# Kernel tuning notes

Measured on AMD Instinct MI355X. Metric: run time of the kernel, lower is better.

Reference implementation:

```python
import jax, jax.numpy as jnp
import numpy as np

B, S, H = 512, 200, 256

def setup_inputs() -> dict:
    key = jax.random.key(0)
    ks = jax.random.split(key, 7)
    scale = 1.0 / np.sqrt(H)
    return {
        "all_memory": jax.random.normal(ks[0], (B, S, H), dtype=jnp.float32),
        "last_memory": jax.random.normal(ks[1], (B, H), dtype=jnp.float32),
        "U": jax.random.normal(ks[2], (H, H), dtype=jnp.float32) * scale,   # U_meta weight
        "W": jax.random.normal(ks[3], (H, H), dtype=jnp.float32) * scale,   # W_meta weight
        "V": jax.random.normal(ks[4], (H, 1), dtype=jnp.float32) * scale,   # V_meta weight (stored as [H,1])
        "MetaW": jax.random.normal(ks[5], (4, H), dtype=jnp.float32) * scale,  # Meta weight
        "Metab": jax.random.normal(ks[6], (4,), dtype=jnp.float32) * scale,    # Meta bias ('multiple' mode)
    }

def reference(all_memory, last_memory, U, W, V, MetaW, Metab):
    # U_meta(all_memory): [B,S,H]; W_meta(last_memory): [B,H] broadcast over S
    a = jnp.einsum('bsh,kh->bsk', all_memory, U)
    l = jnp.einsum('bh,kh->bk', last_memory, W)
    # additive attention score: V_meta(tanh(a + l)) -> [B,S]
    scores = jnp.einsum('bsh,h->bs', jnp.tanh(a + l[:, None, :]), V[:, 0])
    alpha = jax.nn.softmax(scores, axis=1)  # softmax over seq dim
    pooled = jnp.einsum('bs,bsh->bh', alpha, all_memory)  # weighted sum of values
    return pooled @ MetaW.T + Metab  # [B, 4]
```

## Files before the change

### kernel.cpp

```cpp
#include <hip/hip_runtime.h>
#include <hip/hip_bf16.h>
#include <math.h>

#define NB 512
#define NS 200
#define NH 256
#define TILE_S 32
#define NTILES ((NS + TILE_S - 1) / TILE_S)
#define LDSPAD 8
#define LDW (NH + LDSPAD)

typedef __bf16 bf16x8 __attribute__((ext_vector_type(8)));
typedef float  f32x4  __attribute__((ext_vector_type(4)));

__device__ __forceinline__ float tanh_fast(float x) {
  float xc = fminf(fmaxf(x, -10.f), 10.f);
  float e  = __expf(2.f * xc);
  return (e - 1.f) / (e + 1.f);
}

__global__ __launch_bounds__(256, 2)
void fused_meta_attn(const float* __restrict__ mem,
                     const float* __restrict__ lastm,
                     const float* __restrict__ U,
                     const float* __restrict__ W,
                     const float* __restrict__ V,
                     const float* __restrict__ MetaW,
                     const float* __restrict__ Metab,
                     float* __restrict__ out)
{
  const int b    = blockIdx.x;
  const int t    = threadIdx.x;
  const int wave = t >> 6;
  const int lane = t & 63;
  const int m16  = lane & 15;
  const int quad = lane >> 4;

  __shared__ __align__(16) __bf16 mem_sm[TILE_S][LDW];
  __shared__ float lm_sm[NH];
  __shared__ float l_sm[NH];
  __shared__ float v_sm[NH];
  __shared__ float swave_sm[4][TILE_S];
  __shared__ float scores_sm[TILE_S];
  __shared__ float pooled_sm[NH];

  lm_sm[t] = lastm[(size_t)b * NH + t];
  v_sm[t]  = V[t];
  __syncthreads();

  {
    const float4* wrow = (const float4*)(W + (size_t)t * NH);
    const float4* lrow = (const float4*)lm_sm;
    float a0 = 0.f, a1 = 0.f, a2 = 0.f, a3 = 0.f;
#pragma unroll 8
    for (int i = 0; i < NH / 4; ++i) {
      float4 w4 = wrow[i];
      float4 m4 = lrow[i];
      a0 = fmaf(w4.x, m4.x, a0);
      a1 = fmaf(w4.y, m4.y, a1);
      a2 = fmaf(w4.z, m4.z, a2);
      a3 = fmaf(w4.w, m4.w, a3);
    }
    l_sm[t] = (a0 + a1) + (a2 + a3);
  }

  bf16x8 u_frag[4][8];
#pragma unroll
  for (int nf = 0; nf < 4; ++nf) {
    const int n = wave * 64 + nf * 16 + m16;
    const float* urow = U + (size_t)n * NH;
#pragma unroll
    for (int kk = 0; kk < 8; ++kk) {
      const float4 lo = *(const float4*)(urow + kk * 32 + quad * 8);
      const float4 hi = *(const float4*)(urow + kk * 32 + quad * 8 + 4);
      bf16x8 f;
      f[0] = (__bf16)lo.x; f[1] = (__bf16)lo.y;
      f[2] = (__bf16)lo.z; f[3] = (__bf16)lo.w;
      f[4] = (__bf16)hi.x; f[5] = (__bf16)hi.y;
      f[6] = (__bf16)hi.z; f[7] = (__bf16)hi.w;
      u_frag[nf][kk] = f;
    }
  }

  float m_run  = -INFINITY;
  float Z      = 0.f;
  float pooled = 0.f;

  __syncthreads();

  float l_reg[4], v_reg[4];
#pragma unroll
  for (int nf = 0; nf < 4; ++nf) {
    const int n = wave * 64 + nf * 16 + m16;
    l_reg[nf] = l_sm[n];
    v_reg[nf] = v_sm[n];
  }

  for (int tile = 0; tile < NTILES; ++tile) {
    const int s0   = tile * TILE_S;
    const int rows = min(TILE_S, NS - s0);

    const float4* src = (const float4*)(mem + ((size_t)b * NS + s0) * NH);
#pragma unroll
    for (int i = 0; i < (TILE_S * NH / 4) / 256; ++i) {
      const int f   = i * 256 + t;
      const int row = f >> 6;
      const int c4  = (f & 63) * 4;
      float4 v4;
      if (row < rows) v4 = src[f];
      else            v4 = make_float4(0.f, 0.f, 0.f, 0.f);
      __bf16* dst = &mem_sm[row][c4];
      dst[0] = (__bf16)v4.x; dst[1] = (__bf16)v4.y;
      dst[2] = (__bf16)v4.z; dst[3] = (__bf16)v4.w;
    }
    __syncthreads();

    f32x4 acc[2][4];
    const f32x4 fzero = {0.f, 0.f, 0.f, 0.f};
#pragma unroll
    for (int mt = 0; mt < 2; ++mt)
#pragma unroll
      for (int nf = 0; nf < 4; ++nf)
        acc[mt][nf] = fzero;

#pragma unroll
    for (int kk = 0; kk < 8; ++kk) {
      const int c = kk * 32 + quad * 8;
      bf16x8 a0 = *(const bf16x8*)&mem_sm[m16][c];
      bf16x8 a1 = *(const bf16x8*)&mem_sm[16 + m16][c];
#pragma unroll
      for (int nf = 0; nf < 4; ++nf) {
        acc[0][nf] = __builtin_amdgcn_mfma_f32_16x16x32_bf16(a0, u_frag[nf][kk], acc[0][nf], 0, 0, 0);
        acc[1][nf] = __builtin_amdgcn_mfma_f32_16x16x32_bf16(a1, u_frag[nf][kk], acc[1][nf], 0, 0, 0);
      }
    }

    float p[2][4];
#pragma unroll
    for (int mt = 0; mt < 2; ++mt) {
#pragma unroll
      for (int reg = 0; reg < 4; ++reg) {
        float s = 0.f;
#pragma unroll
        for (int nf = 0; nf < 4; ++nf)
          s = fmaf(tanh_fast(acc[mt][nf][reg] + l_reg[nf]), v_reg[nf], s);
        p[mt][reg] = s;
      }
    }
#pragma unroll
    for (int off = 1; off < 16; off <<= 1) {
#pragma unroll
      for (int mt = 0; mt < 2; ++mt)
#pragma unroll
        for (int reg = 0; reg < 4; ++reg)
          p[mt][reg] += __shfl_xor(p[mt][reg], off);
    }
    if (m16 == 0) {
#pragma unroll
      for (int mt = 0; mt < 2; ++mt)
#pragma unroll
        for (int reg = 0; reg < 4; ++reg)
          swave_sm[wave][mt * 16 + quad * 4 + reg] = p[mt][reg];
    }
    __syncthreads();

    if (t < TILE_S)
      scores_sm[t] = swave_sm[0][t] + swave_sm[1][t] + swave_sm[2][t] + swave_sm[3][t];
    __syncthreads();

    float m_tile = -INFINITY;
    for (int r = 0; r < rows; ++r) m_tile = fmaxf(m_tile, scores_sm[r]);
    const float m_new = fmaxf(m_run, m_tile);
    const float fac   = __expf(m_run - m_new);
    float z_t = 0.f, pool_t = 0.f;
    for (int r = 0; r < rows; ++r) {
      const float e = __expf(scores_sm[r] - m_new);
      z_t += e;
      pool_t = fmaf(e, (float)mem_sm[r][t], pool_t);
    }
    Z      = Z * fac + z_t;
    pooled = pooled * fac + pool_t;
    m_run  = m_new;
    __syncthreads();
  }

  pooled_sm[t] = pooled / Z;
  __syncthreads();

  float s = 0.f;
#pragma unroll
  for (int i = 0; i < 4; ++i) {
    const int h = i * 64 + lane;
    s = fmaf(pooled_sm[h], MetaW[(size_t)wave * NH + h], s);
  }
#pragma unroll
  for (int off = 32; off > 0; off >>= 1)
    s += __shfl_down(s, off);
  if (lane == 0)
    out[b * 4 + wave] = s + Metab[wave];
}

extern "C" void kernel_launch(void* const* d_in, const int* in_sizes, int n_in,
                              void* d_out, int out_size, void* d_ws, size_t ws_size,
                              hipStream_t stream) {
  const float* mem   = (const float*)d_in[0];
  const float* lastm = (const float*)d_in[1];
  const float* U     = (const float*)d_in[2];
  const float* W     = (const float*)d_in[3];
  const float* V     = (const float*)d_in[4];
  const float* MetaW = (const float*)d_in[5];
  const float* Metab = (const float*)d_in[6];
  float* out = (float*)d_out;

  hipLaunchKernelGGL(fused_meta_attn, dim3(NB), dim3(256), 0, stream,
                     mem, lastm, U, W, V, MetaW, Metab, out);
}
```

Before: 226.9 us.

## Split sequence across two blocks per batch with a separate softmax merge kernel

Each batch row is now handled by two blocks, one covering the first 96 positions and one covering the remaining 104. Each block writes its partial max, normalizer and pooled vector to workspace, and a second kernel merges the two partials and applies the final projection. The aim is more blocks in flight and shorter serial tile loops, at the cost of recomputing the W projection and U fragments twice per batch and adding a second launch. Tile loads also now pack 8 bf16 values into one LDS store, and launch bounds ask for 4 blocks per CU.

```diff
diff --git a/kernel.cpp b/kernel.cpp
--- a/kernel.cpp
+++ b/kernel.cpp
@@ -6,9 +6,9 @@
 #define NS 200
 #define NH 256
 #define TILE_S 32
-#define NTILES ((NS + TILE_S - 1) / TILE_S)
 #define LDSPAD 8
 #define LDW (NH + LDSPAD)
+#define WS_STRIDE 258
 
 typedef __bf16 bf16x8 __attribute__((ext_vector_type(8)));
 typedef float  f32x4  __attribute__((ext_vector_type(4)));
@@ -19,17 +19,20 @@
   return (e - 1.f) / (e + 1.f);
 }
 
-__global__ __launch_bounds__(256, 2)
-void fused_meta_attn(const float* __restrict__ mem,
-                     const float* __restrict__ lastm,
-                     const float* __restrict__ U,
-                     const float* __restrict__ W,
-                     const float* __restrict__ V,
-                     const float* __restrict__ MetaW,
-                     const float* __restrict__ Metab,
-                     float* __restrict__ out)
+__global__ __launch_bounds__(256, 4)
+void fused_meta_attn_part(const float* __restrict__ mem,
+                          const float* __restrict__ lastm,
+                          const float* __restrict__ U,
+                          const float* __restrict__ W,
+                          const float* __restrict__ V,
+                          float* __restrict__ ws)
 {
-  const int b    = blockIdx.x;
+  const int b    = blockIdx.x >> 1;
+  const int half = blockIdx.x & 1;
+  const int s_begin = half ? 96 : 0;
+  const int s_end   = half ? NS : 96;
+  const int ntiles  = half ? 4 : 3;
+
   const int t    = threadIdx.x;
   const int wave = t >> 6;
   const int lane = t & 63;
@@ -42,7 +45,6 @@
   __shared__ float v_sm[NH];
   __shared__ float swave_sm[4][TILE_S];
   __shared__ float scores_sm[TILE_S];
-  __shared__ float pooled_sm[NH];
 
   lm_sm[t] = lastm[(size_t)b * NH + t];
   v_sm[t]  = V[t];
@@ -96,22 +98,28 @@
     v_reg[nf] = v_sm[n];
   }
 
-  for (int tile = 0; tile < NTILES; ++tile) {
-    const int s0   = tile * TILE_S;
-    const int rows = min(TILE_S, NS - s0);
-
-    const float4* src = (const float4*)(mem + ((size_t)b * NS + s0) * NH);
-#pragma unroll
-    for (int i = 0; i < (TILE_S * NH / 4) / 256; ++i) {
-      const int f   = i * 256 + t;
-      const int row = f >> 6;
-      const int c4  = (f & 63) * 4;
-      float4 v4;
-      if (row < rows) v4 = src[f];
-      else            v4 = make_float4(0.f, 0.f, 0.f, 0.f);
-      __bf16* dst = &mem_sm[row][c4];
-      dst[0] = (__bf16)v4.x; dst[1] = (__bf16)v4.y;
-      dst[2] = (__bf16)v4.z; dst[3] = (__bf16)v4.w;
+  for (int tile = 0; tile < ntiles; ++tile) {
+    const int s0   = s_begin + tile * TILE_S;
+    const int rows = min(TILE_S, s_end - s0);
+
+    const float4* src4 = (const float4*)(mem + ((size_t)b * NS + s0) * NH);
+#pragma unroll
+    for (int i = 0; i < 4; ++i) {
+      const int f2  = i * 256 + t;
+      const int row = f2 >> 5;
+      const int c8  = (f2 & 31) * 8;
+      bf16x8 pk;
+      if (row < rows) {
+        const float4 a = src4[f2 * 2];
+        const float4 c = src4[f2 * 2 + 1];
+        pk[0] = (__bf16)a.x; pk[1] = (__bf16)a.y;
+        pk[2] = (__bf16)a.z; pk[3] = (__bf16)a.w;
+        pk[4] = (__bf16)c.x; pk[5] = (__bf16)c.y;
+        pk[6] = (__bf16)c.z; pk[7] = (__bf16)c.w;
+      } else {
+        pk = (bf16x8)(__bf16)0.f;
+      }
+      *(bf16x8*)&mem_sm[row][c8] = pk;
     }
     __syncthreads();
 
@@ -184,7 +192,34 @@
     __syncthreads();
   }
 
-  pooled_sm[t] = pooled / Z;
+  float* base = ws + (size_t)blockIdx.x * WS_STRIDE;
+  if (t == 0) { base[0] = m_run; base[1] = Z; }
+  base[2 + t] = pooled;
+}
+
+__global__ __launch_bounds__(256, 4)
+void merge_project(const float* __restrict__ ws,
+                   const float* __restrict__ MetaW,
+                   const float* __restrict__ Metab,
+                   float* __restrict__ out)
+{
+  const int b    = blockIdx.x;
+  const int t    = threadIdx.x;
+  const int wave = t >> 6;
+  const int lane = t & 63;
+
+  __shared__ float pooled_sm[NH];
+
+  const float* b0 = ws + (size_t)(b * 2)     * WS_STRIDE;
+  const float* b1 = ws + (size_t)(b * 2 + 1) * WS_STRIDE;
+  const float m0 = b0[0], Z0 = b0[1];
+  const float m1 = b1[0], Z1 = b1[1];
+  const float mm = fmaxf(m0, m1);
+  const float w0 = __expf(m0 - mm);
+  const float w1 = __expf(m1 - mm);
+  const float Zi = 1.f / (Z0 * w0 + Z1 * w1);
+
+  pooled_sm[t] = (b0[2 + t] * w0 + b1[2 + t] * w1) * Zi;
   __syncthreads();
 
   float s = 0.f;
@@ -211,7 +246,10 @@
   const float* MetaW = (const float*)d_in[5];
   const float* Metab = (const float*)d_in[6];
   float* out = (float*)d_out;
-
-  hipLaunchKernelGGL(fused_meta_attn, dim3(NB), dim3(256), 0, stream,
-                     mem, lastm, U, W, V, MetaW, Metab, out);
-}
+  float* ws  = (float*)d_ws;
+
+  hipLaunchKernelGGL(fused_meta_attn_part, dim3(NB * 2), dim3(256), 0, stream,
+                     mem, lastm, U, W, V, ws);
+  hipLaunchKernelGGL(merge_project, dim3(NB), dim3(256), 0, stream,
+                     ws, MetaW, Metab, out);
+}
```

Result: slower. 302.7 us (+33.4%).
